# Performance work log

Measured on AMD Instinct MI355X. Metric: run time of the kernel, lower is better.

The kernel has to match this reference:

```python
import jax, jax.numpy as jnp
import numpy as np

C = 64          # channels
K = 15          # sum(shell_sizes)=1+14
H = 32          # neighbors per query
N = 50000       # support points (== query points M)
RADIUS = 1.0
SIGMA = 0.7
INF = 1e6
BN_EPS = 1e-5


def _init_kernel_points(key):
    # stand-in for load_kernels: 1 center point + 14 points on a sphere shell
    pts = jax.random.normal(key, (K - 1, 3), dtype=jnp.float32)
    pts = pts / jnp.linalg.norm(pts, axis=1, keepdims=True) * RADIUS
    return jnp.concatenate([jnp.zeros((1, 3), jnp.float32), pts], axis=0)


def setup_inputs() -> dict:
    key = jax.random.key(0)
    ks = jax.random.split(key, 10)
    q_pts = jax.random.normal(ks[0], (N, 3), dtype=jnp.float32)
    s_pts = jax.random.normal(ks[1], (N, 3), dtype=jnp.float32)
    s_feats = jax.random.normal(ks[2], (N, C), dtype=jnp.float32)
    neighb_inds = jax.random.randint(ks[3], (N, H), 0, N)
    kernel_points = _init_kernel_points(ks[4])
    # alpha_mlp: Linear(C->C, no bias) -> BatchNorm -> LeakyReLU(0.1) -> Linear(C->K*C)
    lim1 = 1.0 / np.sqrt(C)
    W1 = jax.random.uniform(ks[5], (C, C), jnp.float32, -lim1, lim1)
    gamma = jnp.ones((C,), jnp.float32)
    beta = jnp.zeros((C,), jnp.float32)
    W2 = jax.random.uniform(ks[6], (C, K * C), jnp.float32, -lim1, lim1)
    b2 = jax.random.uniform(ks[7], (K * C,), jnp.float32, -lim1, lim1)
    return {"q_pts": q_pts, "s_pts": s_pts, "s_feats": s_feats,
            "neighb_inds": neighb_inds, "kernel_points": kernel_points,
            "W1": W1, "gamma": gamma, "beta": beta, "W2": W2, "b2": b2}


def reference(q_pts, s_pts, s_feats, neighb_inds, kernel_points, W1, gamma, beta, W2, b2):
    M = q_pts.shape[0]
    # alpha_mlp on pooled (= center) features: (M, C) -> (M, K*C)
    h = s_feats @ W1
    mu = jnp.mean(h, axis=0)
    var = jnp.var(h, axis=0)
    h = (h - mu) / jnp.sqrt(var + BN_EPS) * gamma + beta
    h = jax.nn.leaky_relu(h, 0.1)
    conv_weights = (h @ W2 + b2).reshape(M, K, C)

    # gather neighbor features with a zero padding row (index N -> zeros)
    padded_feats = jnp.concatenate([s_feats, jnp.zeros((1, C), s_feats.dtype)], axis=0)
    neighbor_feats = padded_feats[neighb_inds]                 # (M, H, C)

    # relative neighbor positions with inf padding point
    s_pts_pad = jnp.concatenate([s_pts, jnp.full((1, 3), INF, s_pts.dtype)], axis=0)
    neighbors = s_pts_pad[neighb_inds] - q_pts[:, None, :]     # (M, H, 3)

    # kernel-point influence: nearest kernel point + linear influence
    diff = neighbors[:, :, None, :] - kernel_points            # (M, H, K, 3)
    sq_d = jnp.sum(diff * diff, axis=-1)                       # (M, H, K)
    nn_sq = jnp.min(sq_d, axis=-1)                             # (M, H)
    nn_idx = jnp.argmin(sq_d, axis=-1)                         # (M, H)
    infl = jnp.clip(1.0 - jnp.sqrt(nn_sq) / SIGMA, 0.0)        # (M, H)

    # per-neighbor channel weights from the MLP output, gathered by 1nn kernel point
    nw = jnp.take_along_axis(conv_weights, nn_idx[:, :, None], axis=1)  # (M, H, C)
    nw = nw * infl[:, :, None]

    # weighted aggregation (merge=mul, aggr=sum over neighbors)
    return jnp.sum(neighbor_feats * nw, axis=1)                # (M, C)
```

## Files before the change

### kernel.cpp

```cpp
#include <hip/hip_runtime.h>
#include <hip/hip_bf16.h>
#include <math.h>

#define N_PTS 50000
#define CCH   64
#define KP    15
#define NH    32
#define SIGMA 0.7f
#define BN_EPS 1e-5f
#define LEAKY 0.1f
#define QB    16
#define CWS   18
#define STATS_BLOCKS 1024
#define W2P_BLOCKS   30
#define QC           64
#define CLS_BLOCKS   782
#define PACK_BLOCKS  196

typedef short bf16x8 __attribute__((ext_vector_type(8)));
typedef float floatx4 __attribute__((ext_vector_type(4)));

__device__ __forceinline__ unsigned short f2b(float f) {
    union { float f; unsigned u; } v; v.f = f;
    return (unsigned short)((v.u + 0x7FFFu + ((v.u >> 16) & 1u)) >> 16);
}
__device__ __forceinline__ ushort2 f2b2(float a, float b) {
    __hip_bfloat162 h = __float22bfloat162_rn(float2{a, b});
    union { __hip_bfloat162 h; ushort2 u; } v; v.h = h;
    return v.u;
}
__device__ __forceinline__ float b2f(unsigned short b) {
    union { unsigned u; float f; } v; v.u = ((unsigned)b) << 16;
    return v.f;
}

__global__ __launch_bounds__(256) void k_pack4(const float* __restrict__ sp,
                                               float4* __restrict__ sp4) {
    int i = blockIdx.x * 256 + threadIdx.x;
    if (i < N_PTS) {
        float4 v;
        v.x = sp[i * 3 + 0]; v.y = sp[i * 3 + 1]; v.z = sp[i * 3 + 2]; v.w = 0.f;
        sp4[i] = v;
    }
}

__global__ __launch_bounds__(256) void k_prep(const float* __restrict__ sf,
                                              const float* __restrict__ W1,
                                              const float* __restrict__ W2,
                                              const float* __restrict__ q_pts,
                                              const float4* __restrict__ sp4,
                                              const int* __restrict__ nb,
                                              const float* __restrict__ kpts,
                                              float* __restrict__ bn,
                                              unsigned short* __restrict__ hst,
                                              unsigned short* __restrict__ w2b,
                                              unsigned short* __restrict__ sfb,
                                              unsigned* __restrict__ packG,
                                              int* __restrict__ cntG) {
    int t = threadIdx.x;
    if (blockIdx.x >= STATS_BLOCKS + W2P_BLOCKS) {
        int q0 = (blockIdx.x - (STATS_BLOCKS + W2P_BLOCKS)) * QC;
        int lane = t & 63, lh = lane & 31;
        __shared__ unsigned cbuf[QC * NH];
        __shared__ int      ccnt[QC];

        int idx8[8];
        #pragma unroll
        for (int r = 0; r < 8; ++r) {
            int task = t + r * 256;
            int m = q0 + (task >> 5);
            idx8[r] = (m < N_PTS) ? nb[m * NH + (task & 31)] : 0;
        }
        float4 sv[8]; float qx[8], qy[8], qz[8];
        #pragma unroll
        for (int r = 0; r < 8; ++r) {
            int m = q0 + ((t + r * 256) >> 5);
            int mm = (m < N_PTS) ? m : 0;
            sv[r] = sp4[idx8[r]];
            qx[r] = q_pts[mm * 3 + 0];
            qy[r] = q_pts[mm * 3 + 1];
            qz[r] = q_pts[mm * 3 + 2];
        }
        float kpr[45];
        #pragma unroll
        for (int i = 0; i < 45; ++i) kpr[i] = kpts[i];

        #pragma unroll
        for (int r = 0; r < 8; ++r) {
            int task = t + r * 256;
            int ql = task >> 5;
            bool valid = (q0 + ql < N_PTS);
            float px = sv[r].x - qx[r], py = sv[r].y - qy[r], pz = sv[r].z - qz[r];
            float best = 1e30f; int bi = 0;
            #pragma unroll
            for (int k = 0; k < KP; ++k) {
                float dx = px - kpr[k*3], dy = py - kpr[k*3+1], dz = pz - kpr[k*3+2];
                float d = dx * dx + dy * dy + dz * dz;
                if (d < best) { best = d; bi = k; }
            }
            float infl = 1.f - sqrtf(best) * (1.0f / SIGMA);
            bool act = valid && (infl > 0.f);
            unsigned long long bal = __ballot(act);
            unsigned m32 = (unsigned)(bal >> (lane & 32));
            int prefix = __popc(m32 & ((1u << lh) - 1u));
            int cntq   = __popc(m32);
            int slot   = act ? prefix : cntq + (lh - prefix);
            int iq = (int)(infl * 4095.f + 0.5f);
            unsigned val = act ? ((unsigned)idx8[r] | ((unsigned)bi << 16)
                                  | ((unsigned)iq << 20)) : 0u;
            cbuf[ql * NH + slot] = val;
            if (lh == 0) ccnt[ql] = cntq;
        }
        __syncthreads();
        #pragma unroll
        for (int i = 0; i < 2; ++i) {
            int di = (t + i * 256) * 4;
            if (q0 + (di >> 5) < N_PTS)
                *(uint4*)(packG + q0 * NH + di) = *(const uint4*)(cbuf + di);
        }
        if (t < QC && q0 + t < N_PTS) cntG[q0 + t] = ccnt[t];
        return;
    }
    if (blockIdx.x >= STATS_BLOCKS) {
        int g = (blockIdx.x - STATS_BLOCKS) * 256 + t;
        int lane = g & 63, s = (g >> 6) & 1, tt = g >> 7;
        int col = lane & 15, quad = lane >> 4;
        int base = (s * 32 + quad * 8) * 960 + tt * 16 + col;
        ushort4 lo, hi;
        lo.x = f2b(W2[base + 0 * 960]); lo.y = f2b(W2[base + 1 * 960]);
        lo.z = f2b(W2[base + 2 * 960]); lo.w = f2b(W2[base + 3 * 960]);
        hi.x = f2b(W2[base + 4 * 960]); hi.y = f2b(W2[base + 5 * 960]);
        hi.z = f2b(W2[base + 6 * 960]); hi.w = f2b(W2[base + 7 * 960]);
        *(ushort4*)(w2b + g * 8)     = lo;
        *(ushort4*)(w2b + g * 8 + 4) = hi;
        return;
    }
    int c = t & 63, ml = t >> 6;
    float w1c[64];
    #pragma unroll
    for (int i = 0; i < 64; ++i) w1c[i] = W1[i * 64 + c];
    __shared__ float rows[4][64];
    float acc_s = 0.f, acc_q = 0.f;
    for (int m0 = blockIdx.x * 4; m0 < N_PTS; m0 += STATS_BLOCKS * 4) {
        __syncthreads();
        float v = sf[m0 * 64 + t];
        ((float*)rows)[t] = v;
        sfb[m0 * 64 + t] = f2b(v);
        __syncthreads();
        float h = 0.f;
        #pragma unroll
        for (int i4 = 0; i4 < 16; ++i4) {
            float4 r = *(const float4*)&rows[ml][i4 * 4];
            h += r.x * w1c[i4 * 4] + r.y * w1c[i4 * 4 + 1]
               + r.z * w1c[i4 * 4 + 2] + r.w * w1c[i4 * 4 + 3];
        }
        acc_s += h;
        acc_q += h * h;
        hst[(m0 + ml) * 64 + c] = f2b(h);
    }
    __shared__ float red[2][256];
    red[0][t] = acc_s; red[1][t] = acc_q;
    __syncthreads();
    if (t < 64) {
        float s = red[0][t] + red[0][64 + t] + red[0][128 + t] + red[0][192 + t];
        float q = red[1][t] + red[1][64 + t] + red[1][128 + t] + red[1][192 + t];
        atomicAdd(&bn[t], s);
        atomicAdd(&bn[64 + t], q);
    }
}

__global__ __launch_bounds__(256, 4) void k_main(
    const unsigned short* __restrict__ sfb,
    const float* __restrict__ gamma, const float* __restrict__ beta,
    const float* __restrict__ bn, const float* __restrict__ b2,
    const unsigned short* __restrict__ w2b, const unsigned short* __restrict__ hst,
    const unsigned* __restrict__ packG, const int* __restrict__ cntG,
    float* __restrict__ out) {

    __shared__ __align__(16) unsigned short cwT[960 * CWS];
    __shared__ float abS[128];

    int t = threadIdx.x;
    int lane = t & 63, wv = t >> 6;
    int m0 = blockIdx.x * QB;

    if (t < 64) {
        float mu  = bn[t] * (1.0f / N_PTS);
        float var = bn[64 + t] * (1.0f / N_PTS) - mu * mu;
        float a   = gamma[t] * rsqrtf(var + BN_EPS);
        abS[t]      = a;
        abS[64 + t] = beta[t] - mu * a;
    }
    __syncthreads();

    int row = lane & 15, half = lane >> 4;
    bf16x8 a0, a1;
    {
        const unsigned short* hrow = hst + (m0 + row) * 64 + half * 8;
        bf16x8 r0 = *(const bf16x8*)(hrow);
        bf16x8 r1 = *(const bf16x8*)(hrow + 32);
        #pragma unroll
        for (int j = 0; j < 8; j += 2) {
            int c0 = half * 8 + j;
            float g0 = abS[c0] * b2f((unsigned short)r0[j]) + abS[64 + c0];
            float g1 = abS[c0 + 1] * b2f((unsigned short)r0[j + 1]) + abS[64 + c0 + 1];
            g0 = g0 > 0.f ? g0 : LEAKY * g0;
            g1 = g1 > 0.f ? g1 : LEAKY * g1;
            ushort2 p01 = f2b2(g0, g1);
            a0[j] = (short)p01.x; a0[j + 1] = (short)p01.y;
            int c1 = 32 + c0;
            float g2 = abS[c1] * b2f((unsigned short)r1[j]) + abS[64 + c1];
            float g3 = abS[c1 + 1] * b2f((unsigned short)r1[j + 1]) + abS[64 + c1 + 1];
            g2 = g2 > 0.f ? g2 : LEAKY * g2;
            g3 = g3 > 0.f ? g3 : LEAKY * g3;
            ushort2 p23 = f2b2(g2, g3);
            a1[j] = (short)p23.x; a1[j + 1] = (short)p23.y;
        }
    }

    {
        int col = lane & 15, quad = lane >> 4;
        for (int ti = 0; ti < 15; ++ti) {
            int tt = wv * 15 + ti;
            bf16x8 bf0 = *(const bf16x8*)(w2b + ((tt * 2 + 0) * 64 + lane) * 8);
            bf16x8 bf1 = *(const bf16x8*)(w2b + ((tt * 2 + 1) * 64 + lane) * 8);
            floatx4 acc = {0.f, 0.f, 0.f, 0.f};
            acc = __builtin_amdgcn_mfma_f32_16x16x32_bf16(a0, bf0, acc, 0, 0, 0);
            acc = __builtin_amdgcn_mfma_f32_16x16x32_bf16(a1, bf1, acc, 0, 0, 0);
            int n = tt * 16 + col;
            float bb = b2[n];
            unsigned short* dst = &cwT[n * CWS + quad * 4];
            ushort2 w01 = f2b2(acc[0] + bb, acc[1] + bb);
            ushort2 w23 = f2b2(acc[2] + bb, acc[3] + bb);
            *(ushort2*)(dst)     = w01;
            *(ushort2*)(dst + 2) = w23;
        }
    }
    __syncthreads();

    {
        int wvu = __builtin_amdgcn_readfirstlane(wv);
        int c = lane;
        #pragma unroll
        for (int pp = 0; pp < 2; ++pp) {
            int qa = wvu * 4 + pp * 2, qb = qa + 1;
            int ma = m0 + qa, mb = m0 + qb;
            const unsigned* pA = packG + ma * NH;
            const unsigned* pB = packG + mb * NH;
            const unsigned short* cwa = cwT + c * CWS + qa;
            const unsigned short* cwb = cwa + 1;
            int cA = cntG[ma], cB = cntG[mb];
            int na = cA > cB ? cA : cB;
            na = (na + 3) & ~3;
            float accA = 0.f, accB = 0.f;
            for (int jj = 0; jj < na; jj += 4) {
                unsigned pa0 = pA[jj], pa1 = pA[jj+1], pa2 = pA[jj+2], pa3 = pA[jj+3];
                unsigned pb0 = pB[jj], pb1 = pB[jj+1], pb2 = pB[jj+2], pb3 = pB[jj+3];
                float fA0 = b2f(sfb[(pa0 & 0xFFFFu) * 64 + c]);
                float fA1 = b2f(sfb[(pa1 & 0xFFFFu) * 64 + c]);
                float fA2 = b2f(sfb[(pa2 & 0xFFFFu) * 64 + c]);
                float fA3 = b2f(sfb[(pa3 & 0xFFFFu) * 64 + c]);
                float fB0 = b2f(sfb[(pb0 & 0xFFFFu) * 64 + c]);
                float fB1 = b2f(sfb[(pb1 & 0xFFFFu) * 64 + c]);
                float fB2 = b2f(sfb[(pb2 & 0xFFFFu) * 64 + c]);
                float fB3 = b2f(sfb[(pb3 & 0xFFFFu) * 64 + c]);
                float wA0 = b2f(cwa[((pa0 >> 16) & 15u) * (64 * CWS)]);
                float wA1 = b2f(cwa[((pa1 >> 16) & 15u) * (64 * CWS)]);
                float wA2 = b2f(cwa[((pa2 >> 16) & 15u) * (64 * CWS)]);
                float wA3 = b2f(cwa[((pa3 >> 16) & 15u) * (64 * CWS)]);
                float wB0 = b2f(cwb[((pb0 >> 16) & 15u) * (64 * CWS)]);
                float wB1 = b2f(cwb[((pb1 >> 16) & 15u) * (64 * CWS)]);
                float wB2 = b2f(cwb[((pb2 >> 16) & 15u) * (64 * CWS)]);
                float wB3 = b2f(cwb[((pb3 >> 16) & 15u) * (64 * CWS)]);
                float iA0 = (float)(pa0 >> 20), iA1 = (float)(pa1 >> 20);
                float iA2 = (float)(pa2 >> 20), iA3 = (float)(pa3 >> 20);
                float iB0 = (float)(pb0 >> 20), iB1 = (float)(pb1 >> 20);
                float iB2 = (float)(pb2 >> 20), iB3 = (float)(pb3 >> 20);
                accA += iA0 * fA0 * wA0 + iA1 * fA1 * wA1
                      + iA2 * fA2 * wA2 + iA3 * fA3 * wA3;
                accB += iB0 * fB0 * wB0 + iB1 * fB1 * wB1
                      + iB2 * fB2 * wB2 + iB3 * fB3 * wB3;
            }
            const float qs = 1.f / 4095.f;
            out[ma * 64 + c] = accA * qs;
            out[mb * 64 + c] = accB * qs;
        }
    }
}

extern "C" void kernel_launch(void* const* d_in, const int* in_sizes, int n_in,
                              void* d_out, int out_size, void* d_ws, size_t ws_size,
                              hipStream_t stream) {
    const float* q_pts   = (const float*)d_in[0];
    const float* s_pts   = (const float*)d_in[1];
    const float* s_feats = (const float*)d_in[2];
    const int*   nb      = (const int*)d_in[3];
    const float* kpts    = (const float*)d_in[4];
    const float* W1      = (const float*)d_in[5];
    const float* gamma   = (const float*)d_in[6];
    const float* beta    = (const float*)d_in[7];
    const float* W2      = (const float*)d_in[8];
    const float* b2      = (const float*)d_in[9];
    float* out = (float*)d_out;

    float* ws = (float*)d_ws;
    float* bn = ws;
    unsigned short* w2b = (unsigned short*)(ws + 128);
    unsigned short* hst = w2b + 61440;
    unsigned short* sfb = hst + N_PTS * CCH;
    unsigned* packG = (unsigned*)(sfb + N_PTS * CCH);
    int* cntG = (int*)(packG + N_PTS * NH);
    float4* sp4 = (float4*)(cntG + ((N_PTS + 3) & ~3));

    hipMemsetAsync(bn, 0, 128 * sizeof(float), stream);
    k_pack4<<<PACK_BLOCKS, 256, 0, stream>>>(s_pts, sp4);
    k_prep<<<STATS_BLOCKS + W2P_BLOCKS + CLS_BLOCKS, 256, 0, stream>>>(
        s_feats, W1, W2, q_pts, sp4, nb, kpts, bn, hst, w2b, sfb, packG, cntG);
    k_main<<<N_PTS / QB, 256, 0, stream>>>(sfb, gamma, beta, bn, b2, w2b, hst,
                                           packG, cntG, out);
}
```

Baseline: 163.9 us.

## Restructure prep kernels: fold memset into pack kernel, split stats and classification

Removes the separate memset by zeroing the BN accumulators inside a new k_misc kernel. That kernel also packs support points and transposes W2 to bf16 through shared memory for coalesced reads. The stats kernel now processes 16 rows per iteration with float4 loads and packed bf16 stores, and neighbor classification moves into its own kernel. The launch count stays at four, and separating stats from classification changes the heterogeneous block mix and may reduce overlap between the two phases.

```diff
diff --git a/kernel.cpp b/kernel.cpp
--- a/kernel.cpp
+++ b/kernel.cpp
@@ -12,7 +12,6 @@
 #define QB    16
 #define CWS   18
 #define STATS_BLOCKS 1024
-#define W2P_BLOCKS   30
 #define QC           64
 #define CLS_BLOCKS   782
 #define PACK_BLOCKS  196
@@ -34,129 +33,78 @@
     return v.f;
 }
 
-__global__ __launch_bounds__(256) void k_pack4(const float* __restrict__ sp,
-                                               float4* __restrict__ sp4) {
-    int i = blockIdx.x * 256 + threadIdx.x;
-    if (i < N_PTS) {
-        float4 v;
-        v.x = sp[i * 3 + 0]; v.y = sp[i * 3 + 1]; v.z = sp[i * 3 + 2]; v.w = 0.f;
-        sp4[i] = v;
-    }
-}
-
-__global__ __launch_bounds__(256) void k_prep(const float* __restrict__ sf,
-                                              const float* __restrict__ W1,
+__global__ __launch_bounds__(256) void k_misc(const float* __restrict__ sp,
                                               const float* __restrict__ W2,
-                                              const float* __restrict__ q_pts,
-                                              const float4* __restrict__ sp4,
-                                              const int* __restrict__ nb,
-                                              const float* __restrict__ kpts,
-                                              float* __restrict__ bn,
-                                              unsigned short* __restrict__ hst,
+                                              float4* __restrict__ sp4,
                                               unsigned short* __restrict__ w2b,
-                                              unsigned short* __restrict__ sfb,
-                                              unsigned* __restrict__ packG,
-                                              int* __restrict__ cntG) {
+                                              float* __restrict__ bn) {
     int t = threadIdx.x;
-    if (blockIdx.x >= STATS_BLOCKS + W2P_BLOCKS) {
-        int q0 = (blockIdx.x - (STATS_BLOCKS + W2P_BLOCKS)) * QC;
-        int lane = t & 63, lh = lane & 31;
-        __shared__ unsigned cbuf[QC * NH];
-        __shared__ int      ccnt[QC];
-
-        int idx8[8];
-        #pragma unroll
-        for (int r = 0; r < 8; ++r) {
-            int task = t + r * 256;
-            int m = q0 + (task >> 5);
-            idx8[r] = (m < N_PTS) ? nb[m * NH + (task & 31)] : 0;
-        }
-        float4 sv[8]; float qx[8], qy[8], qz[8];
-        #pragma unroll
-        for (int r = 0; r < 8; ++r) {
-            int m = q0 + ((t + r * 256) >> 5);
-            int mm = (m < N_PTS) ? m : 0;
-            sv[r] = sp4[idx8[r]];
-            qx[r] = q_pts[mm * 3 + 0];
-            qy[r] = q_pts[mm * 3 + 1];
-            qz[r] = q_pts[mm * 3 + 2];
-        }
-        float kpr[45];
-        #pragma unroll
-        for (int i = 0; i < 45; ++i) kpr[i] = kpts[i];
-
-        #pragma unroll
-        for (int r = 0; r < 8; ++r) {
-            int task = t + r * 256;
-            int ql = task >> 5;
-            bool valid = (q0 + ql < N_PTS);
-            float px = sv[r].x - qx[r], py = sv[r].y - qy[r], pz = sv[r].z - qz[r];
-            float best = 1e30f; int bi = 0;
+    if (blockIdx.x >= PACK_BLOCKS + 1) {
+        int tt = blockIdx.x - (PACK_BLOCKS + 1);
+        __shared__ float ld[64 * 16];
+        {
+            int k = t >> 2, colg = t & 3;
+            *(float4*)&ld[k * 16 + colg * 4] =
+                *(const float4*)&W2[k * 960 + tt * 16 + colg * 4];
+        }
+        __syncthreads();
+        if (t < 128) {
+            int s = t >> 6, lane = t & 63;
+            int quad = lane >> 4, col = lane & 15;
+            unsigned short v[8];
             #pragma unroll
-            for (int k = 0; k < KP; ++k) {
-                float dx = px - kpr[k*3], dy = py - kpr[k*3+1], dz = pz - kpr[k*3+2];
-                float d = dx * dx + dy * dy + dz * dz;
-                if (d < best) { best = d; bi = k; }
-            }
-            float infl = 1.f - sqrtf(best) * (1.0f / SIGMA);
-            bool act = valid && (infl > 0.f);
-            unsigned long long bal = __ballot(act);
-            unsigned m32 = (unsigned)(bal >> (lane & 32));
-            int prefix = __popc(m32 & ((1u << lh) - 1u));
-            int cntq   = __popc(m32);
-            int slot   = act ? prefix : cntq + (lh - prefix);
-            int iq = (int)(infl * 4095.f + 0.5f);
-            unsigned val = act ? ((unsigned)idx8[r] | ((unsigned)bi << 16)
-                                  | ((unsigned)iq << 20)) : 0u;
-            cbuf[ql * NH + slot] = val;
-            if (lh == 0) ccnt[ql] = cntq;
-        }
+            for (int j = 0; j < 8; ++j)
+                v[j] = f2b(ld[(s * 32 + quad * 8 + j) * 16 + col]);
+            unsigned short* dst = w2b + ((tt * 2 + s) * 64 + lane) * 8;
+            *(ushort4*)(dst)     = ushort4{v[0], v[1], v[2], v[3]};
+            *(ushort4*)(dst + 4) = ushort4{v[4], v[5], v[6], v[7]};
+        }
+        return;
+    }
+    if (blockIdx.x == 0 && t < 128) bn[t] = 0.f;
+    if (blockIdx.x < PACK_BLOCKS + 1) {
+        int i = blockIdx.x * 256 + t;
+        if (i < N_PTS) {
+            float4 v;
+            v.x = sp[i * 3 + 0]; v.y = sp[i * 3 + 1]; v.z = sp[i * 3 + 2]; v.w = 0.f;
+            sp4[i] = v;
+        }
+    }
+}
+
+__global__ __launch_bounds__(256) void k_stats(const float* __restrict__ sf,
+                                               const float* __restrict__ W1,
+                                               float* __restrict__ bn,
+                                               unsigned short* __restrict__ hst,
+                                               unsigned short* __restrict__ sfb) {
+    int t = threadIdx.x;
+    int c = t & 63, rg = t >> 6;
+    float w1c[64];
+    #pragma unroll
+    for (int i = 0; i < 64; ++i) w1c[i] = W1[i * 64 + c];
+    __shared__ float ld[16 * 64];
+    float acc_s = 0.f, acc_q = 0.f;
+    for (int m0 = blockIdx.x * 16; m0 < N_PTS; m0 += STATS_BLOCKS * 16) {
+        __syncthreads();
+        float4 v = *(const float4*)&sf[m0 * 64 + t * 4];
+        *(float4*)&ld[t * 4] = v;
+        ushort2 lo = f2b2(v.x, v.y), hi = f2b2(v.z, v.w);
+        *(ushort4*)&sfb[m0 * 64 + t * 4] = ushort4{lo.x, lo.y, hi.x, hi.y};
         __syncthreads();
         #pragma unroll
-        for (int i = 0; i < 2; ++i) {
-            int di = (t + i * 256) * 4;
-            if (q0 + (di >> 5) < N_PTS)
-                *(uint4*)(packG + q0 * NH + di) = *(const uint4*)(cbuf + di);
-        }
-        if (t < QC && q0 + t < N_PTS) cntG[q0 + t] = ccnt[t];
-        return;
-    }
-    if (blockIdx.x >= STATS_BLOCKS) {
-        int g = (blockIdx.x - STATS_BLOCKS) * 256 + t;
-        int lane = g & 63, s = (g >> 6) & 1, tt = g >> 7;
-        int col = lane & 15, quad = lane >> 4;
-        int base = (s * 32 + quad * 8) * 960 + tt * 16 + col;
-        ushort4 lo, hi;
-        lo.x = f2b(W2[base + 0 * 960]); lo.y = f2b(W2[base + 1 * 960]);
-        lo.z = f2b(W2[base + 2 * 960]); lo.w = f2b(W2[base + 3 * 960]);
-        hi.x = f2b(W2[base + 4 * 960]); hi.y = f2b(W2[base + 5 * 960]);
-        hi.z = f2b(W2[base + 6 * 960]); hi.w = f2b(W2[base + 7 * 960]);
-        *(ushort4*)(w2b + g * 8)     = lo;
-        *(ushort4*)(w2b + g * 8 + 4) = hi;
-        return;
-    }
-    int c = t & 63, ml = t >> 6;
-    float w1c[64];
-    #pragma unroll
-    for (int i = 0; i < 64; ++i) w1c[i] = W1[i * 64 + c];
-    __shared__ float rows[4][64];
-    float acc_s = 0.f, acc_q = 0.f;
-    for (int m0 = blockIdx.x * 4; m0 < N_PTS; m0 += STATS_BLOCKS * 4) {
-        __syncthreads();
-        float v = sf[m0 * 64 + t];
-        ((float*)rows)[t] = v;
-        sfb[m0 * 64 + t] = f2b(v);
-        __syncthreads();
-        float h = 0.f;
-        #pragma unroll
-        for (int i4 = 0; i4 < 16; ++i4) {
-            float4 r = *(const float4*)&rows[ml][i4 * 4];
-            h += r.x * w1c[i4 * 4] + r.y * w1c[i4 * 4 + 1]
-               + r.z * w1c[i4 * 4 + 2] + r.w * w1c[i4 * 4 + 3];
-        }
-        acc_s += h;
-        acc_q += h * h;
-        hst[(m0 + ml) * 64 + c] = f2b(h);
+        for (int rr = 0; rr < 4; ++rr) {
+            int r = rg + rr * 4;
+            float h = 0.f;
+            #pragma unroll
+            for (int i4 = 0; i4 < 16; ++i4) {
+                float4 rv = *(const float4*)&ld[r * 64 + i4 * 4];
+                h += rv.x * w1c[i4 * 4] + rv.y * w1c[i4 * 4 + 1]
+                   + rv.z * w1c[i4 * 4 + 2] + rv.w * w1c[i4 * 4 + 3];
+            }
+            acc_s += h;
+            acc_q += h * h;
+            hst[(m0 + r) * 64 + c] = f2b(h);
+        }
     }
     __shared__ float red[2][256];
     red[0][t] = acc_s; red[1][t] = acc_q;
@@ -167,6 +115,75 @@
         atomicAdd(&bn[t], s);
         atomicAdd(&bn[64 + t], q);
     }
+}
+
+__global__ __launch_bounds__(256, 4) void k_cls(const float* __restrict__ q_pts,
+                                                const float4* __restrict__ sp4,
+                                                const int* __restrict__ nb,
+                                                const float* __restrict__ kpts,
+                                                unsigned* __restrict__ packG,
+                                                int* __restrict__ cntG) {
+    int t = threadIdx.x;
+    int q0 = blockIdx.x * QC;
+    int lane = t & 63, lh = lane & 31;
+    __shared__ unsigned cbuf[QC * NH];
+    __shared__ int      ccnt[QC];
+
+    int idx8[8];
+    #pragma unroll
+    for (int r = 0; r < 8; ++r) {
+        int task = t + r * 256;
+        int m = q0 + (task >> 5);
+        idx8[r] = (m < N_PTS) ? nb[m * NH + (task & 31)] : 0;
+    }
+    float4 sv[8]; float qx[8], qy[8], qz[8];
+    #pragma unroll
+    for (int r = 0; r < 8; ++r) {
+        int m = q0 + ((t + r * 256) >> 5);
+        int mm = (m < N_PTS) ? m : 0;
+        sv[r] = sp4[idx8[r]];
+        qx[r] = q_pts[mm * 3 + 0];
+        qy[r] = q_pts[mm * 3 + 1];
+        qz[r] = q_pts[mm * 3 + 2];
+    }
+    float kpr[45];
+    #pragma unroll
+    for (int i = 0; i < 45; ++i) kpr[i] = kpts[i];
+
+    #pragma unroll
+    for (int r = 0; r < 8; ++r) {
+        int task = t + r * 256;
+        int ql = task >> 5;
+        bool valid = (q0 + ql < N_PTS);
+        float px = sv[r].x - qx[r], py = sv[r].y - qy[r], pz = sv[r].z - qz[r];
+        float best = 1e30f; int bi = 0;
+        #pragma unroll
+        for (int k = 0; k < KP; ++k) {
+            float dx = px - kpr[k*3], dy = py - kpr[k*3+1], dz = pz - kpr[k*3+2];
+            float d = dx * dx + dy * dy + dz * dz;
+            if (d < best) { best = d; bi = k; }
+        }
+        float infl = 1.f - sqrtf(best) * (1.0f / SIGMA);
+        bool act = valid && (infl > 0.f);
+        unsigned long long bal = __ballot(act);
+        unsigned m32 = (unsigned)(bal >> (lane & 32));
+        int prefix = __popc(m32 & ((1u << lh) - 1u));
+        int cntq   = __popc(m32);
+        int slot   = act ? prefix : cntq + (lh - prefix);
+        int iq = (int)(infl * 4095.f + 0.5f);
+        unsigned val = act ? ((unsigned)idx8[r] | ((unsigned)bi << 16)
+                              | ((unsigned)iq << 20)) : 0u;
+        cbuf[ql * NH + slot] = val;
+        if (lh == 0) ccnt[ql] = cntq;
+    }
+    __syncthreads();
+    #pragma unroll
+    for (int i = 0; i < 2; ++i) {
+        int di = (t + i * 256) * 4;
+        if (q0 + (di >> 5) < N_PTS)
+            *(uint4*)(packG + q0 * NH + di) = *(const uint4*)(cbuf + di);
+    }
+    if (t < QC && q0 + t < N_PTS) cntG[q0 + t] = ccnt[t];
 }
 
 __global__ __launch_bounds__(256, 4) void k_main(
@@ -312,10 +329,9 @@
     int* cntG = (int*)(packG + N_PTS * NH);
     float4* sp4 = (float4*)(cntG + ((N_PTS + 3) & ~3));
 
-    hipMemsetAsync(bn, 0, 128 * sizeof(float), stream);
-    k_pack4<<<PACK_BLOCKS, 256, 0, stream>>>(s_pts, sp4);
-    k_prep<<<STATS_BLOCKS + W2P_BLOCKS + CLS_BLOCKS, 256, 0, stream>>>(
-        s_feats, W1, W2, q_pts, sp4, nb, kpts, bn, hst, w2b, sfb, packG, cntG);
+    k_misc<<<PACK_BLOCKS + 1 + 60, 256, 0, stream>>>(s_pts, W2, sp4, w2b, bn);
+    k_stats<<<STATS_BLOCKS, 256, 0, stream>>>(s_feats, W1, bn, hst, sfb);
+    k_cls<<<CLS_BLOCKS, 256, 0, stream>>>(q_pts, sp4, nb, kpts, packG, cntG);
     k_main<<<N_PTS / QB, 256, 0, stream>>>(sfb, gamma, beta, bn, b2, w2b, hst,
                                            packG, cntG, out);
 }
```

Result: no change. 162.9 us (-0.6%).
